# Performance work log

Hardware: AMD Instinct MI355X
Metric: run time of the kernel (lower is better)

## Reference

```python
import jax, jax.numpy as jnp
import numpy as np

EPS = 1e-8


def setup_inputs() -> dict:
    key = jax.random.key(0)
    k1, k2, k3, k4 = jax.random.split(key, 4)
    B, C, H, W = 16, 256, 32, 32
    E, V = 512, 8192
    x = jax.random.normal(k1, (B, C, H, W), dtype=jnp.float32)
    w_pre = jax.random.normal(k2, (E, C), dtype=jnp.float32) * 0.05
    b_pre = jax.random.normal(k3, (E,), dtype=jnp.float32) * 0.05
    # embedding init mirrors uniform_(-1/vocab, 1/vocab)
    embedding = jax.random.uniform(k4, (V, E), dtype=jnp.float32, minval=-1.0 / V, maxval=1.0 / V)
    return {"x": x, "w_pre": w_pre, "b_pre": b_pre, "embedding": embedding}


def reference(x, w_pre, b_pre, embedding):
    B, C, H, W = x.shape
    V, E = embedding.shape
    # pre_quant_conv: 1x1 Conv2d == per-pixel linear over channels
    z = jnp.einsum('bchw,ec->behw', x, w_pre) + b_pre[None, :, None, None]  # [B,E,H,W]
    # flatten to (b h w, e)
    z_flat = z.transpose(0, 2, 3, 1).reshape(-1, E)  # [BHW, E]
    zn = z_flat / (EPS + jnp.linalg.norm(z_flat, axis=1, keepdims=True))
    en = embedding / (EPS + jnp.linalg.norm(embedding, axis=1, keepdims=True))
    sims = zn @ en.T  # [BHW, V]
    tokens = jnp.argmax(sims, axis=-1)  # [BHW]
    z_q = embedding[tokens].reshape(B, H, W, E).transpose(0, 3, 1, 2)  # [B,E,H,W]
    # straight-through norm-blend from Tokenizer.forward
    normed_z = z / (EPS + jnp.linalg.norm(z, axis=1, keepdims=True))
    norm_zq = EPS + jnp.linalg.norm(z_q, axis=1, keepdims=True)
    normed_zq = z_q / norm_zq
    decoder_input = (normed_z + jax.lax.stop_gradient(normed_zq - normed_z)) * norm_zq
    return z, z_q, decoder_input, tokens.reshape(B, H * W)
```

## Files before the change

kernel.cpp:

```cpp
#include <hip/hip_runtime.h>
#include <math.h>

#define EPSF 1e-8f
#define MARGIN 4e-3f

constexpr int Bn = 16, Cc = 256, HW = 1024, Ee = 512, Vv = 8192;
constexpr int Mm = Bn * HW;

constexpr long O_Z   = 0;
constexpr long O_ZQ  = 8388608;
constexpr long O_DEC = 16777216;
constexpr long O_TOK = 25165824;

typedef __attribute__((ext_vector_type(8))) short s16x8;
typedef __attribute__((ext_vector_type(4))) short s16x4;
typedef __attribute__((ext_vector_type(8))) _Float16 f16x8;
typedef __attribute__((ext_vector_type(4))) float f32x4;

__device__ __forceinline__ unsigned short f2h(float x) {
    _Float16 h = (_Float16)x;
    return __builtin_bit_cast(unsigned short, h);
}
__device__ __forceinline__ float h2f(unsigned short b) {
    return (float)__builtin_bit_cast(_Float16, b);
}


__global__ void k_wT(const float* __restrict__ w, float* __restrict__ wT) {
    int gid = blockIdx.x * 256 + threadIdx.x;
    int c = gid >> 9, e = gid & 511;
    wT[gid] = w[e * Cc + c];
}

__global__ void k_en(const float* __restrict__ emb, float* __restrict__ en_inv,
                     float* __restrict__ en_norm) {
    int v = blockIdx.x * 4 + (threadIdx.x >> 6);
    int lane = threadIdx.x & 63;
    const float* row = emb + (long)v * Ee;
    float s = 0.f;
#pragma unroll
    for (int j = 0; j < 8; ++j) { float xv = row[lane + 64 * j]; s += xv * xv; }
#pragma unroll
    for (int off = 32; off; off >>= 1) s += __shfl_xor(s, off);
    if (lane == 0) {
        float n = sqrtf(s);
        en_norm[v] = EPSF + n;
        en_inv[v]  = 1.0f / (EPSF + n);
    }
}


__global__ __launch_bounds__(256) void k_gemm1(const float* __restrict__ x,
                                               const float* __restrict__ wT,
                                               const float* __restrict__ bias,
                                               float* __restrict__ z) {
    __shared__ float As[32][64];
    __shared__ float Bs[32][64];
    int m0 = blockIdx.x * 64;
    int b = m0 >> 10, hw0 = m0 & 1023;
    int e0 = blockIdx.y * 64;
    int t = threadIdx.x;
    int mi = t >> 4, ni = t & 15;
    float acc[4][4] = {};
    for (int c0 = 0; c0 < Cc; c0 += 32) {
#pragma unroll
        for (int q = 0; q < 2; ++q) {
            int f = t + 256 * q;
            int kk = f >> 4, m4 = (f & 15) * 4;
            *(float4*)&As[kk][m4] = *(const float4*)(x + ((long)(b * Cc + c0 + kk)) * HW + hw0 + m4);
            *(float4*)&Bs[kk][m4] = *(const float4*)(wT + (long)(c0 + kk) * Ee + e0 + m4);
        }
        __syncthreads();
#pragma unroll
        for (int kk = 0; kk < 32; ++kk) {
            float4 a = *(float4*)&As[kk][mi * 4];
            float4 bv = *(float4*)&Bs[kk][ni * 4];
            float av[4] = {a.x, a.y, a.z, a.w};
            float bb[4] = {bv.x, bv.y, bv.z, bv.w};
#pragma unroll
            for (int r = 0; r < 4; ++r)
#pragma unroll
                for (int c = 0; c < 4; ++c) acc[r][c] = fmaf(av[r], bb[c], acc[r][c]);
        }
        __syncthreads();
    }
#pragma unroll
    for (int c = 0; c < 4; ++c) {
        int e = e0 + ni * 4 + c;
        float be = bias[e];
        float4 o = make_float4(acc[0][c] + be, acc[1][c] + be, acc[2][c] + be, acc[3][c] + be);
        *(float4*)(z + ((long)(b * Ee + e)) * HW + hw0 + mi * 4) = o;
    }
}

__global__ void k_znorm(const float* __restrict__ z, float* __restrict__ inv_zn) {
    __shared__ float partial[4][64];
    int lp = threadIdx.x & 63;
    int q = threadIdx.x >> 6;
    int p = blockIdx.x * 64 + lp;
    int b = p >> 10, hw = p & 1023;
    const float* base = z + ((long)(b * Ee + q * 128)) * HW + hw;
    float s = 0.f;
    for (int e = 0; e < 128; ++e) { float xv = base[(long)e * HW]; s = fmaf(xv, xv, s); }
    partial[q][lp] = s;
    __syncthreads();
    if (threadIdx.x < 64) {
        float t = ((partial[0][threadIdx.x] + partial[1][threadIdx.x]) +
                   partial[2][threadIdx.x]) + partial[3][threadIdx.x];
        inv_zn[blockIdx.x * 64 + threadIdx.x] = 1.0f / (EPSF + sqrtf(t));
    }
}


__global__ void k_Asplit(const float* __restrict__ z, const float* __restrict__ inv_zn,
                         unsigned short* __restrict__ Ahi, unsigned short* __restrict__ Alo) {
    __shared__ float tile[64][65];
    int p0 = (blockIdx.x >> 3) * 64;
    int e0 = (blockIdx.x & 7) * 64;
    int b = p0 >> 10, hw0 = p0 & 1023;
    int t = threadIdx.x;
#pragma unroll
    for (int q = 0; q < 4; ++q) {
        int f = t + 256 * q;
        int e_l = f >> 4, p4 = (f & 15) * 4;
        float4 d = *(const float4*)(z + ((long)(b * Ee + e0 + e_l)) * HW + hw0 + p4);
        tile[e_l][p4 + 0] = d.x; tile[e_l][p4 + 1] = d.y;
        tile[e_l][p4 + 2] = d.z; tile[e_l][p4 + 3] = d.w;
    }
    __syncthreads();
#pragma unroll
    for (int q = 0; q < 4; ++q) {
        int f = t + 256 * q;
        int p_l = f >> 4, e4 = (f & 15) * 4;
        float inv = inv_zn[p0 + p_l];
        s16x4 h, lo;
#pragma unroll
        for (int j = 0; j < 4; ++j) {
            float xv = tile[e4 + j][p_l] * inv;
            unsigned short hh = f2h(xv);
            h[j]  = (short)hh;
            lo[j] = (short)f2h(xv - h2f(hh));
        }
        long off = (long)(p0 + p_l) * Ee + e0 + e4;
        *(s16x4*)(Ahi + off) = h;
        *(s16x4*)(Alo + off) = lo;
    }
}


__global__ void k_Bh(const float* __restrict__ emb, const float* __restrict__ en_inv,
                     unsigned short* __restrict__ Bhi) {
    int gid = blockIdx.x * 256 + threadIdx.x;
    int v = gid >> 7, c4 = (gid & 127) * 4;
    float inv = en_inv[v];
    float4 d = *(const float4*)(emb + (long)v * Ee + c4);
    s16x4 h;
    h[0] = (short)f2h(d.x * inv); h[1] = (short)f2h(d.y * inv);
    h[2] = (short)f2h(d.z * inv); h[3] = (short)f2h(d.w * inv);
    *(s16x4*)(Bhi + (long)v * Ee + c4) = h;
}


__global__ __launch_bounds__(256, 2) void k_sims(const unsigned short* __restrict__ Ahi,
                                                 const unsigned short* __restrict__ Bhi,
                                                 float* __restrict__ part_v,
                                                 int* __restrict__ part_i,
                                                 float2* __restrict__ extras,
                                                 int* __restrict__ cnt) {
    __shared__ short As[128 * 64];
    __shared__ short Bs[128 * 64];
    __shared__ float red_v[2][2][64];
    __shared__ int   red_i[2][2][64];
    __shared__ float red_m[2][64];
    __shared__ int   red_wi[2][64];

    int t = threadIdx.x;
    int wg = blockIdx.x;
    int xcd = wg & 7, r = wg >> 3;
    int bx = xcd * 16 + (r & 15);
    int by = r >> 4;
    long m0 = (long)bx * 128, n0 = (long)by * 128;

    int wid = t >> 6, l = t & 63;
    int wr = wid >> 1, wc = wid & 1;
    int srow = t >> 3, sslot = t & 7;
    int l15 = l & 15, lg = l >> 4;

    f32x4 acc[4][4];
#pragma unroll
    for (int i = 0; i < 4; ++i)
#pragma unroll
        for (int j = 0; j < 4; ++j) acc[i][j] = (f32x4){0.f, 0.f, 0.f, 0.f};

    for (int kt = 0; kt < 8; ++kt) {
        int k0 = kt * 64;
        s16x8 ra[4], rb[4];
#pragma unroll
        for (int q = 0; q < 4; ++q) {
            int rr = srow + 32 * q;
            ra[q] = *(const s16x8*)(Ahi + (m0 + rr) * Ee + k0 + sslot * 8);
            rb[q] = *(const s16x8*)(Bhi + (n0 + rr) * Ee + k0 + sslot * 8);
        }
        __syncthreads();
#pragma unroll
        for (int q = 0; q < 4; ++q) {
            int rr = srow + 32 * q;
            int sw = (sslot ^ (rr & 7)) * 8;
            *(s16x8*)&As[rr * 64 + sw] = ra[q];
            *(s16x8*)&Bs[rr * 64 + sw] = rb[q];
        }
        __syncthreads();
        s16x8 af[4][2], bf[4][2];
#pragma unroll
        for (int mt = 0; mt < 4; ++mt)
#pragma unroll
            for (int kk = 0; kk < 2; ++kk) {
                int row = wr * 64 + mt * 16 + l15;
                int g = kk * 4 + lg;
                af[mt][kk] = *(s16x8*)&As[row * 64 + ((g ^ (row & 7)) * 8)];
                int nrow = wc * 64 + mt * 16 + l15;
                bf[mt][kk] = *(s16x8*)&Bs[nrow * 64 + ((g ^ (nrow & 7)) * 8)];
            }
#pragma unroll
        for (int kk = 0; kk < 2; ++kk)
#pragma unroll
            for (int mt = 0; mt < 4; ++mt)
#pragma unroll
                for (int nt = 0; nt < 4; ++nt)
                    acc[mt][nt] = __builtin_amdgcn_mfma_f32_16x16x32_f16(
                        __builtin_bit_cast(f16x8, af[mt][kk]),
                        __builtin_bit_cast(f16x8, bf[nt][kk]), acc[mt][nt], 0, 0, 0);
    }

#pragma unroll
    for (int mt = 0; mt < 4; ++mt)
#pragma unroll
        for (int rg = 0; rg < 4; ++rg) {
            float best = -3e38f; int bi = 0x7FFFFFFF;
#pragma unroll
            for (int nt = 0; nt < 4; ++nt) {
                float val = acc[mt][nt][rg];
                int idx = (int)n0 + wc * 64 + nt * 16 + l15;
                if (val > best) { best = val; bi = idx; }
            }
#pragma unroll
            for (int off = 1; off < 16; off <<= 1) {
                float ov = __shfl_xor(best, off);
                int oi = __shfl_xor(bi, off);
                if (ov > best || (ov == best && oi < bi)) { best = ov; bi = oi; }
            }
            if (l15 == 0) {
                int rloc = mt * 16 + lg * 4 + rg;
                red_v[wr][wc][rloc] = best;
                red_i[wr][wc][rloc] = bi;
            }
        }
    __syncthreads();
    if (t < 128) {
        int wr_ = t >> 6, rloc = t & 63;
        float va = red_v[wr_][0][rloc]; int ia = red_i[wr_][0][rloc];
        float vb = red_v[wr_][1][rloc]; int ib = red_i[wr_][1][rloc];
        if (vb > va || (vb == va && ib < ia)) { va = vb; ia = ib; }
        long m = m0 + wr_ * 64 + rloc;
        part_v[m * 64 + by] = va;
        part_i[m * 64 + by] = ia;
        red_m[wr_][rloc] = va;
        red_wi[wr_][rloc] = ia;
    }
    __syncthreads();
#pragma unroll
    for (int mt = 0; mt < 4; ++mt)
#pragma unroll
        for (int rg = 0; rg < 4; ++rg) {
            int rloc = mt * 16 + lg * 4 + rg;
            float bm = red_m[wr][rloc];
            int wi_ = red_wi[wr][rloc];
            long p = m0 + wr * 64 + rloc;
            float thr = bm - MARGIN;
#pragma unroll
            for (int nt = 0; nt < 4; ++nt) {
                float val = acc[mt][nt][rg];
                int idx = (int)n0 + wc * 64 + nt * 16 + l15;
                if (val >= thr && idx != wi_) {
                    int slot = atomicAdd(&cnt[p], 1);
                    if (slot < 64) extras[p * 64 + slot] = make_float2(val, __int_as_float(idx));
                }
            }
        }
}


__global__ __launch_bounds__(256) void k_pick(const float* __restrict__ part_v,
                                              const int* __restrict__ part_i,
                                              const float2* __restrict__ extras,
                                              const int* __restrict__ cnt,
                                              const unsigned short* __restrict__ Ahi,
                                              const unsigned short* __restrict__ Alo,
                                              const float* __restrict__ emb,
                                              const float* __restrict__ en_inv,
                                              int* __restrict__ tok_i,
                                              float* __restrict__ tok_f) {
    int p = blockIdx.x * 4 + (threadIdx.x >> 6);
    int lane = threadIdx.x & 63;
    float wv = part_v[(long)p * 64 + lane];
    int wi = part_i[(long)p * 64 + lane];
    float m1 = wv;
#pragma unroll
    for (int off = 1; off < 64; off <<= 1) {
        float ov = __shfl_xor(m1, off);
        if (ov > m1) m1 = ov;
    }
    float thr = m1 - MARGIN;
    int n = cnt[p]; if (n > 64) n = 64;
    float ev = -3e38f; int ei = 0;
    if (lane < n) {
        float2 e2 = extras[(long)p * 64 + lane];
        ev = e2.x; ei = __float_as_int(e2.y);
    }
    unsigned long long mw = __ballot(wv >= thr);
    unsigned long long me = __ballot(ev >= thr);
    s16x8 ah = *(const s16x8*)(Ahi + (long)p * Ee + lane * 8);
    s16x8 al = *(const s16x8*)(Alo + (long)p * Ee + lane * 8);
    float a[8];
#pragma unroll
    for (int j = 0; j < 8; ++j)
        a[j] = h2f((unsigned short)ah[j]) + h2f((unsigned short)al[j]);

    float best = -3e38f; int bi = 0x7FFFFFFF;
    auto rescore = [&](int v) {
        const float* er = emb + (long)v * Ee + lane * 8;
        float4 b0 = *(const float4*)er;
        float4 b1 = *(const float4*)(er + 4);
        float s = 0.f;
        s = fmaf(a[0], b0.x, s); s = fmaf(a[1], b0.y, s);
        s = fmaf(a[2], b0.z, s); s = fmaf(a[3], b0.w, s);
        s = fmaf(a[4], b1.x, s); s = fmaf(a[5], b1.y, s);
        s = fmaf(a[6], b1.z, s); s = fmaf(a[7], b1.w, s);
#pragma unroll
        for (int off = 1; off < 64; off <<= 1) s += __shfl_xor(s, off);
        s *= en_inv[v];
        if (s > best || (s == best && v < bi)) { best = s; bi = v; }
    };
    while (mw) {
        int b = __ffsll(mw) - 1; mw &= mw - 1;
        rescore(__shfl(wi, b));
    }
    while (me) {
        int b = __ffsll(me) - 1; me &= me - 1;
        rescore(__shfl(ei, b));
    }
    if (lane == 0) { tok_i[p] = bi; tok_f[p] = (float)bi; }
}


__global__ void k_final(const float* __restrict__ z, const float* __restrict__ emb,
                        const int* __restrict__ tok, const float* __restrict__ inv_zn,
                        const float* __restrict__ en_inv, const float* __restrict__ en_norm,
                        float* __restrict__ zq, float* __restrict__ dec) {
    long gid = (long)blockIdx.x * 256 + threadIdx.x;
    int hw = (int)(gid & 1023);
    int b  = (int)(gid >> 19);
    int p  = (b << 10) | hw;
    int e  = (int)((gid >> 10) & 511);
    int tk = tok[p];
    float zqv = emb[(long)tk * Ee + e];
    float nq  = en_norm[tk];
    float nzq = zqv * en_inv[tk];
    float zv  = z[gid];
    float nz  = zv * inv_zn[p];
    zq[gid]  = zqv;
    dec[gid] = (nz + (nzq - nz)) * nq;
}


extern "C" void kernel_launch(void* const* d_in, const int* in_sizes, int n_in,
                              void* d_out, int out_size, void* d_ws, size_t ws_size,
                              hipStream_t stream) {
    const float* x     = (const float*)d_in[0];
    const float* w_pre = (const float*)d_in[1];
    const float* b_pre = (const float*)d_in[2];
    const float* emb   = (const float*)d_in[3];

    float* out  = (float*)d_out;
    float* z    = out + O_Z;
    float* zq   = out + O_ZQ;
    float* dec  = out + O_DEC;
    float* tokf = out + O_TOK;

    unsigned short* Ahi = (unsigned short*)zq;
    unsigned short* Alo = Ahi + (long)Mm * Ee;
    unsigned short* Bhi = (unsigned short*)dec;
    float*  part_v = dec + 2 * 1024 * 1024;
    int*    part_i = (int*)(dec + 3 * 1024 * 1024);
    float2* extras = (float2*)(dec + 4 * 1024 * 1024);
    int*    cnt    = (int*)(dec + 6 * 1024 * 1024);

    float* ws      = (float*)d_ws;
    float* wT      = ws;
    float* en_inv  = wT + 131072;
    float* en_norm = en_inv + 8192;
    float* inv_zn  = en_norm + 8192;
    int*   tok_i   = (int*)(inv_zn + 16384);

    k_wT<<<512, 256, 0, stream>>>(w_pre, wT);
    k_en<<<2048, 256, 0, stream>>>(emb, en_inv, en_norm);
    dim3 g1(Mm / 64, Ee / 64);
    k_gemm1<<<g1, 256, 0, stream>>>(x, wT, b_pre, z);
    k_znorm<<<Mm / 64, 256, 0, stream>>>(z, inv_zn);
    k_Asplit<<<2048, 256, 0, stream>>>(z, inv_zn, Ahi, Alo);
    k_Bh<<<4096, 256, 0, stream>>>(emb, en_inv, Bhi);
    hipMemsetAsync((void*)cnt, 0, Mm * sizeof(int), stream);
    k_sims<<<8192, 256, 0, stream>>>(Ahi, Bhi, part_v, part_i, extras, cnt);
    k_pick<<<Mm / 4, 256, 0, stream>>>(part_v, part_i, extras, cnt, Ahi, Alo, emb,
                                       en_inv, tok_i, tokf);
    k_final<<<(int)(8388608 / 256), 256, 0, stream>>>(z, emb, tok_i, inv_zn, en_inv, en_norm, zq, dec);
}
```

Measured before the change: 426.4 us.

## Fuse norm passes into producers and double-buffer sims GEMM with direct LDS loads

Merges the embedding norm and fp16 conversion into one kernel, and moves the z row sum-of-squares into the projection GEMM epilogue as per-tile partials that the split kernel reduces. This removes the separate znorm and Bh kernels and their extra passes over z and the embedding. The similarity GEMM now double-buffers its LDS tiles and fills them with global_load_lds, so the next K-tile loads while the current one computes, at the cost of twice the LDS per block. Because the partial sums are added in a different order, the norm rounding changes slightly, which could flip near-tie argmax results.

```diff
diff --git a/kernel.cpp b/kernel.cpp
--- a/kernel.cpp
+++ b/kernel.cpp
@@ -32,28 +32,37 @@
     wT[gid] = w[e * Cc + c];
 }
 
-__global__ void k_en(const float* __restrict__ emb, float* __restrict__ en_inv,
-                     float* __restrict__ en_norm) {
+__global__ void k_enB(const float* __restrict__ emb, float* __restrict__ en_inv,
+                      float* __restrict__ en_norm, unsigned short* __restrict__ Bhi) {
     int v = blockIdx.x * 4 + (threadIdx.x >> 6);
     int lane = threadIdx.x & 63;
-    const float* row = emb + (long)v * Ee;
+    const float* row = emb + (long)v * Ee + lane * 8;
+    float4 d0 = *(const float4*)row;
+    float4 d1 = *(const float4*)(row + 4);
     float s = 0.f;
-#pragma unroll
-    for (int j = 0; j < 8; ++j) { float xv = row[lane + 64 * j]; s += xv * xv; }
+    s = fmaf(d0.x, d0.x, s); s = fmaf(d0.y, d0.y, s);
+    s = fmaf(d0.z, d0.z, s); s = fmaf(d0.w, d0.w, s);
+    s = fmaf(d1.x, d1.x, s); s = fmaf(d1.y, d1.y, s);
+    s = fmaf(d1.z, d1.z, s); s = fmaf(d1.w, d1.w, s);
 #pragma unroll
     for (int off = 32; off; off >>= 1) s += __shfl_xor(s, off);
-    if (lane == 0) {
-        float n = sqrtf(s);
-        en_norm[v] = EPSF + n;
-        en_inv[v]  = 1.0f / (EPSF + n);
-    }
+    float n = sqrtf(s);
+    float inv = 1.0f / (EPSF + n);
+    if (lane == 0) { en_norm[v] = EPSF + n; en_inv[v] = inv; }
+    s16x8 h;
+    h[0] = (short)f2h(d0.x * inv); h[1] = (short)f2h(d0.y * inv);
+    h[2] = (short)f2h(d0.z * inv); h[3] = (short)f2h(d0.w * inv);
+    h[4] = (short)f2h(d1.x * inv); h[5] = (short)f2h(d1.y * inv);
+    h[6] = (short)f2h(d1.z * inv); h[7] = (short)f2h(d1.w * inv);
+    *(s16x8*)(Bhi + (long)v * Ee + lane * 8) = h;
 }
 
 
 __global__ __launch_bounds__(256) void k_gemm1(const float* __restrict__ x,
                                                const float* __restrict__ wT,
                                                const float* __restrict__ bias,
-                                               float* __restrict__ z) {
+                                               float* __restrict__ z,
+                                               float* __restrict__ sumsq_part) {
     __shared__ float As[32][64];
     __shared__ float Bs[32][64];
     int m0 = blockIdx.x * 64;
@@ -84,41 +93,44 @@
         }
         __syncthreads();
     }
+    float sq[4] = {0.f, 0.f, 0.f, 0.f};
 #pragma unroll
     for (int c = 0; c < 4; ++c) {
         int e = e0 + ni * 4 + c;
         float be = bias[e];
         float4 o = make_float4(acc[0][c] + be, acc[1][c] + be, acc[2][c] + be, acc[3][c] + be);
         *(float4*)(z + ((long)(b * Ee + e)) * HW + hw0 + mi * 4) = o;
-    }
-}
-
-__global__ void k_znorm(const float* __restrict__ z, float* __restrict__ inv_zn) {
-    __shared__ float partial[4][64];
-    int lp = threadIdx.x & 63;
-    int q = threadIdx.x >> 6;
-    int p = blockIdx.x * 64 + lp;
-    int b = p >> 10, hw = p & 1023;
-    const float* base = z + ((long)(b * Ee + q * 128)) * HW + hw;
-    float s = 0.f;
-    for (int e = 0; e < 128; ++e) { float xv = base[(long)e * HW]; s = fmaf(xv, xv, s); }
-    partial[q][lp] = s;
-    __syncthreads();
-    if (threadIdx.x < 64) {
-        float t = ((partial[0][threadIdx.x] + partial[1][threadIdx.x]) +
-                   partial[2][threadIdx.x]) + partial[3][threadIdx.x];
-        inv_zn[blockIdx.x * 64 + threadIdx.x] = 1.0f / (EPSF + sqrtf(t));
-    }
-}
-
-
-__global__ void k_Asplit(const float* __restrict__ z, const float* __restrict__ inv_zn,
-                         unsigned short* __restrict__ Ahi, unsigned short* __restrict__ Alo) {
+        sq[0] = fmaf(o.x, o.x, sq[0]); sq[1] = fmaf(o.y, o.y, sq[1]);
+        sq[2] = fmaf(o.z, o.z, sq[2]); sq[3] = fmaf(o.w, o.w, sq[3]);
+    }
+#pragma unroll
+    for (int r = 0; r < 4; ++r)
+#pragma unroll
+        for (int off = 1; off < 16; off <<= 1) sq[r] += __shfl_xor(sq[r], off);
+    if (ni == 0) {
+#pragma unroll
+        for (int r = 0; r < 4; ++r)
+            sumsq_part[(long)(m0 + mi * 4 + r) * 8 + blockIdx.y] = sq[r];
+    }
+}
+
+
+__global__ void k_Asplit(const float* __restrict__ z, const float* __restrict__ sumsq_part,
+                         unsigned short* __restrict__ Ahi, unsigned short* __restrict__ Alo,
+                         float* __restrict__ inv_zn) {
     __shared__ float tile[64][65];
+    __shared__ float inv_s[64];
     int p0 = (blockIdx.x >> 3) * 64;
     int e0 = (blockIdx.x & 7) * 64;
     int b = p0 >> 10, hw0 = p0 & 1023;
     int t = threadIdx.x;
+    if (t < 64) {
+        const float* sp = sumsq_part + (long)(p0 + t) * 8;
+        float s = ((sp[0] + sp[1]) + (sp[2] + sp[3])) + ((sp[4] + sp[5]) + (sp[6] + sp[7]));
+        float inv = 1.0f / (EPSF + sqrtf(s));
+        inv_s[t] = inv;
+        if ((blockIdx.x & 7) == 0) inv_zn[p0 + t] = inv;
+    }
 #pragma unroll
     for (int q = 0; q < 4; ++q) {
         int f = t + 256 * q;
@@ -132,7 +144,7 @@
     for (int q = 0; q < 4; ++q) {
         int f = t + 256 * q;
         int p_l = f >> 4, e4 = (f & 15) * 4;
-        float inv = inv_zn[p0 + p_l];
+        float inv = inv_s[p_l];
         s16x4 h, lo;
 #pragma unroll
         for (int j = 0; j < 4; ++j) {
@@ -145,19 +157,6 @@
         *(s16x4*)(Ahi + off) = h;
         *(s16x4*)(Alo + off) = lo;
     }
-}
-
-
-__global__ void k_Bh(const float* __restrict__ emb, const float* __restrict__ en_inv,
-                     unsigned short* __restrict__ Bhi) {
-    int gid = blockIdx.x * 256 + threadIdx.x;
-    int v = gid >> 7, c4 = (gid & 127) * 4;
-    float inv = en_inv[v];
-    float4 d = *(const float4*)(emb + (long)v * Ee + c4);
-    s16x4 h;
-    h[0] = (short)f2h(d.x * inv); h[1] = (short)f2h(d.y * inv);
-    h[2] = (short)f2h(d.z * inv); h[3] = (short)f2h(d.w * inv);
-    *(s16x4*)(Bhi + (long)v * Ee + c4) = h;
 }
 
 
@@ -167,8 +166,8 @@
                                                  int* __restrict__ part_i,
                                                  float2* __restrict__ extras,
                                                  int* __restrict__ cnt) {
-    __shared__ short As[128 * 64];
-    __shared__ short Bs[128 * 64];
+    __shared__ short As[2][8192];
+    __shared__ short Bs[2][8192];
     __shared__ float red_v[2][2][64];
     __shared__ int   red_i[2][2][64];
     __shared__ float red_m[2][64];
@@ -183,33 +182,38 @@
 
     int wid = t >> 6, l = t & 63;
     int wr = wid >> 1, wc = wid & 1;
-    int srow = t >> 3, sslot = t & 7;
     int l15 = l & 15, lg = l >> 4;
 
+    auto stage = [&](const unsigned short* gbase, short* region, long row0, int k0) {
+#pragma unroll
+        for (int j = 0; j < 4; ++j) {
+            int i = j * 256 + t;
+            int rr = i >> 3, s = i & 7;
+            int sp = s ^ (rr & 7);
+            const unsigned short* gp = gbase + (row0 + rr) * Ee + k0 + sp * 8;
+            short* lp = region + (long)(j * 256 + (t & ~63)) * 8;
+            __builtin_amdgcn_global_load_lds(
+                (const __attribute__((address_space(1))) unsigned int*)gp,
+                (__attribute__((address_space(3))) unsigned int*)lp, 16, 0, 0);
+        }
+    };
+
     f32x4 acc[4][4];
 #pragma unroll
     for (int i = 0; i < 4; ++i)
 #pragma unroll
         for (int j = 0; j < 4; ++j) acc[i][j] = (f32x4){0.f, 0.f, 0.f, 0.f};
 
+    stage(Ahi, &As[0][0], m0, 0);
+    stage(Bhi, &Bs[0][0], n0, 0);
+
     for (int kt = 0; kt < 8; ++kt) {
-        int k0 = kt * 64;
-        s16x8 ra[4], rb[4];
-#pragma unroll
-        for (int q = 0; q < 4; ++q) {
-            int rr = srow + 32 * q;
-            ra[q] = *(const s16x8*)(Ahi + (m0 + rr) * Ee + k0 + sslot * 8);
-            rb[q] = *(const s16x8*)(Bhi + (n0 + rr) * Ee + k0 + sslot * 8);
-        }
+        int cur = kt & 1;
         __syncthreads();
-#pragma unroll
-        for (int q = 0; q < 4; ++q) {
-            int rr = srow + 32 * q;
-            int sw = (sslot ^ (rr & 7)) * 8;
-            *(s16x8*)&As[rr * 64 + sw] = ra[q];
-            *(s16x8*)&Bs[rr * 64 + sw] = rb[q];
-        }
-        __syncthreads();
+        if (kt < 7) {
+            stage(Ahi, &As[cur ^ 1][0], m0, (kt + 1) * 64);
+            stage(Bhi, &Bs[cur ^ 1][0], n0, (kt + 1) * 64);
+        }
         s16x8 af[4][2], bf[4][2];
 #pragma unroll
         for (int mt = 0; mt < 4; ++mt)
@@ -217,9 +221,9 @@
             for (int kk = 0; kk < 2; ++kk) {
                 int row = wr * 64 + mt * 16 + l15;
                 int g = kk * 4 + lg;
-                af[mt][kk] = *(s16x8*)&As[row * 64 + ((g ^ (row & 7)) * 8)];
+                af[mt][kk] = *(const s16x8*)&As[cur][row * 64 + ((g ^ (row & 7)) * 8)];
                 int nrow = wc * 64 + mt * 16 + l15;
-                bf[mt][kk] = *(s16x8*)&Bs[nrow * 64 + ((g ^ (nrow & 7)) * 8)];
+                bf[mt][kk] = *(const s16x8*)&Bs[cur][nrow * 64 + ((g ^ (nrow & 7)) * 8)];
             }
 #pragma unroll
         for (int kk = 0; kk < 2; ++kk)
@@ -394,6 +398,7 @@
     int*    part_i = (int*)(dec + 3 * 1024 * 1024);
     float2* extras = (float2*)(dec + 4 * 1024 * 1024);
     int*    cnt    = (int*)(dec + 6 * 1024 * 1024);
+    float*  sumsq_part = dec + 6 * 1024 * 1024 + 32768;
 
     float* ws      = (float*)d_ws;
     float* wT      = ws;
@@ -403,12 +408,10 @@
     int*   tok_i   = (int*)(inv_zn + 16384);
 
     k_wT<<<512, 256, 0, stream>>>(w_pre, wT);
-    k_en<<<2048, 256, 0, stream>>>(emb, en_inv, en_norm);
+    k_enB<<<2048, 256, 0, stream>>>(emb, en_inv, en_norm, Bhi);
     dim3 g1(Mm / 64, Ee / 64);
-    k_gemm1<<<g1, 256, 0, stream>>>(x, wT, b_pre, z);
-    k_znorm<<<Mm / 64, 256, 0, stream>>>(z, inv_zn);
-    k_Asplit<<<2048, 256, 0, stream>>>(z, inv_zn, Ahi, Alo);
-    k_Bh<<<4096, 256, 0, stream>>>(emb, en_inv, Bhi);
+    k_gemm1<<<g1, 256, 0, stream>>>(x, wT, b_pre, z, sumsq_part);
+    k_Asplit<<<2048, 256, 0, stream>>>(z, sumsq_part, Ahi, Alo, inv_zn);
     hipMemsetAsync((void*)cnt, 0, Mm * sizeof(int), stream);
     k_sims<<<8192, 256, 0, stream>>>(Ahi, Bhi, part_v, part_i, extras, cnt);
     k_pick<<<Mm / 4, 256, 0, stream>>>(part_v, part_i, extras, cnt, Ahi, Alo, emb,
```

Result: slower. 517.2 us (+21.3%).
